# Optimization experiments

Hardware: AMD Instinct MI355X
Metric: run time of the kernel (lower is better)

The kernel has to match this reference:

```python
import jax, jax.numpy as jnp
import numpy as np

N_NODES = 50000
N_EDGES = 800000
D_IN = 128
HC = 128
D_OUT = 128
BN_EPS = 1e-5
RRELU_SLOPE = (1.0 / 8.0 + 1.0 / 3.0) / 2.0  # RReLU eval mode: (lower+upper)/2 = 11/48


def setup_inputs() -> dict:
    key = jax.random.key(0)
    ks = jax.random.split(key, 10)
    s_in = 1.0 / np.sqrt(D_IN)
    s_hc = 1.0 / np.sqrt(HC)
    return {
        "x": jax.random.normal(ks[0], (N_NODES, D_IN), jnp.float32),
        "edge_index": jax.random.randint(ks[1], (2, N_EDGES), 0, N_NODES),
        "edge_attr": jax.random.uniform(ks[2], (N_EDGES,), jnp.float32),
        # conv1: GraphConv(D_IN -> HC): lin_rel (with bias) + lin_root (no bias)
        "W1_rel": jax.random.normal(ks[3], (HC, D_IN), jnp.float32) * s_in,
        "b1": jnp.zeros((HC,), jnp.float32),
        "W1_root": jax.random.normal(ks[4], (HC, D_IN), jnp.float32) * s_in,
        # bn1 affine params
        "gamma": jnp.ones((HC,), jnp.float32),
        "beta": jnp.zeros((HC,), jnp.float32),
        # conv2: GraphConv(HC -> D_OUT)
        "W2_rel": jax.random.normal(ks[5], (D_OUT, HC), jnp.float32) * s_hc,
        "b2": jnp.zeros((D_OUT,), jnp.float32),
        "W2_root": jax.random.normal(ks[6], (D_OUT, HC), jnp.float32) * s_hc,
    }


def graph_conv(x, src, tgt, edge_w, W_rel, b_rel, W_root):
    # message: edge_weight * x[src]; aggregate: scatter-add into target nodes
    msg = x[src] * edge_w[:, None]                                   # [E, F]
    agg = jax.ops.segment_sum(msg, tgt, num_segments=x.shape[0])     # [N, F]
    return agg @ W_rel.T + b_rel + x @ W_root.T                      # [N, F_out]


def reference(x, edge_index, edge_attr, W1_rel, b1, W1_root, gamma, beta, W2_rel, b2, W2_root):
    src, tgt = edge_index[0], edge_index[1]
    h = graph_conv(x, src, tgt, edge_attr, W1_rel, b1, W1_root)      # [N, HC]
    # BatchNorm1d (training mode: biased batch stats over node dim)
    mean = h.mean(axis=0)
    var = h.var(axis=0)
    h = (h - mean) * jax.lax.rsqrt(var + BN_EPS) * gamma + beta
    # RReLU (deterministic eval slope)
    h = jnp.where(h >= 0, h, h * RRELU_SLOPE)
    return graph_conv(h, src, tgt, edge_attr, W2_rel, b2, W2_root)   # [N, D_OUT]
```

## Files before the change

kernel.cpp:

```cpp
#include <hip/hip_runtime.h>

#define N_NODES 50000
#define N_EDGES 800000
#define F 128
#define BN_EPS 1e-5f
#define SLOPE 0.22916666666666666f

#define NBKT 196
#define BKT_CAP 8192
#define P1_CHUNK 4096
#define P1_EPB 16
#define P1_BLKS 196
#define CASTX_BLKS 6250
#define CASTW_BLKS 64
#define BKT_FINAL_CAP 9984
#define REC_CAP 1160192
#define N_TILES 3125
#define GG_GRID 2048

typedef __attribute__((ext_vector_type(8))) short bf16x8;
typedef __attribute__((ext_vector_type(4))) float f32x4;
typedef unsigned long long u64;

__device__ __forceinline__ float bf2f(ushort u) {
    union { uint i; float f; } v; v.i = (uint)u << 16; return v.f;
}
__device__ __forceinline__ ushort f2bf(float f) {
    union { float f; uint i; } v; v.f = f;
    uint r = v.i + 0x7fffu + ((v.i >> 16) & 1u);
    return (ushort)(r >> 16);
}

__global__ __launch_bounds__(256) void s1p_k(const int* __restrict__ src,
        const int* __restrict__ tgt, const float* __restrict__ ew,
        int* __restrict__ bcur, u64* __restrict__ stg,
        const float* __restrict__ x, ushort* __restrict__ xb,
        const float* __restrict__ W1r, const float* __restrict__ W1t,
        const float* __restrict__ W2r, const float* __restrict__ W2t,
        ushort* __restrict__ wb) {
    const int b = blockIdx.x;
    if (b >= P1_BLKS) {
        if (b < P1_BLKS + CASTX_BLKS) {
            int i = (b - P1_BLKS) * 256 + threadIdx.x;
            float4 v = reinterpret_cast<const float4*>(x)[i];
            ushort4 o;
            o.x = f2bf(v.x); o.y = f2bf(v.y); o.z = f2bf(v.z); o.w = f2bf(v.w);
            reinterpret_cast<ushort4*>(xb)[i] = o;
        } else {
            int i = (b - P1_BLKS - CASTX_BLKS) * 256 + threadIdx.x;
            int m = i >> 12;
            int j = i & 4095;
            const float* sp = (m == 0) ? W1r : (m == 1) ? W1t : (m == 2) ? W2r : W2t;
            float4 v = reinterpret_cast<const float4*>(sp)[j];
            ushort4 o;
            o.x = f2bf(v.x); o.y = f2bf(v.y); o.z = f2bf(v.z); o.w = f2bf(v.w);
            reinterpret_cast<ushort4*>(wb)[i] = o;
        }
        return;
    }
    __shared__ uint cnt[256];
    __shared__ uint base[256];
    __shared__ uint lcur[256];
    __shared__ uint gbase[256];
    __shared__ u64 lrec[P1_CHUNK];

    const int e0 = b * P1_CHUNK;
    const int nE = min(P1_CHUNK, N_EDGES - e0);
    cnt[threadIdx.x] = 0;
    __syncthreads();

    u64 myrec[P1_EPB];
    bool myok[P1_EPB];
#pragma unroll
    for (int k = 0; k < P1_EPB; ++k) {
        int idx = threadIdx.x + (k << 8);
        bool ok = idx < nE;
        myok[k] = ok;
        if (ok) {
            int e = e0 + idx;
            uint t = (uint)tgt[e];
            uint lo = (uint)(ushort)src[e] | ((uint)f2bf(ew[e]) << 16);
            myrec[k] = (u64)lo | ((u64)t << 32);
            atomicAdd(&cnt[t >> 8], 1u);
        }
    }
    __syncthreads();
    uint v = cnt[threadIdx.x];
    base[threadIdx.x] = v;
    __syncthreads();
    for (int o = 1; o < 256; o <<= 1) {
        uint t = (threadIdx.x >= (unsigned)o) ? base[threadIdx.x - o] : 0;
        __syncthreads();
        base[threadIdx.x] += t;
        __syncthreads();
    }
    uint excl = base[threadIdx.x] - v;
    base[threadIdx.x] = excl;
    lcur[threadIdx.x] = excl;
    if (threadIdx.x < NBKT && v > 0)
        gbase[threadIdx.x] = (uint)threadIdx.x * BKT_CAP +
                             (uint)atomicAdd(&bcur[threadIdx.x], (int)v);
    __syncthreads();
#pragma unroll
    for (int k = 0; k < P1_EPB; ++k) {
        if (myok[k]) {
            uint bb = (uint)(myrec[k] >> 40);
            uint slot = atomicAdd(&lcur[bb], 1u);
            lrec[slot] = myrec[k];
        }
    }
    __syncthreads();
    for (int s = threadIdx.x; s < nE; s += 256) {
        u64 r = lrec[s];
        uint bb = (uint)(r >> 40);
        stg[gbase[bb] + ((uint)s - base[bb])] = r;
    }
}

__global__ __launch_bounds__(256) void sort2_k(const int* __restrict__ bcur,
        const u64* __restrict__ stg, uint* __restrict__ recs, int2* __restrict__ rng) {
    __shared__ int lcnt[256];
    __shared__ int lcur[256];
    __shared__ int sc[256];
    __shared__ int fbase_s;
    __shared__ uint lrec[BKT_FINAL_CAP];
    const int b = blockIdx.x;
    const int tid = threadIdx.x;

    int cnt_t = (tid < NBKT) ? bcur[tid] : 0;
    int stride_t = (tid < NBKT) ? (((cnt_t + 7) & ~7) + 1792) : 0;
    sc[tid] = stride_t;
    lcnt[tid] = 0;
    __syncthreads();
    for (int o = 1; o < 256; o <<= 1) {
        int t = (tid >= o) ? sc[tid - o] : 0;
        __syncthreads();
        sc[tid] += t;
        __syncthreads();
    }
    if (tid == b) fbase_s = sc[tid] - stride_t;
    __syncthreads();
    const int fbase = fbase_s;
    const int cnt = bcur[b];
    const u64* sb = stg + (size_t)b * BKT_CAP;

    for (int i = tid; i < cnt; i += 256)
        atomicAdd(&lcnt[(int)(sb[i] >> 32) & 255], 1);
    __syncthreads();
    const int node = b * 256 + tid;
    int myc = lcnt[tid];
    int myp = (myc + 7) & ~7;
    if (node >= N_NODES) myp = 0;
    sc[tid] = myp;
    __syncthreads();
    for (int o = 1; o < 256; o <<= 1) {
        int t = (tid >= o) ? sc[tid - o] : 0;
        __syncthreads();
        sc[tid] += t;
        __syncthreads();
    }
    const int myoff = sc[tid] - myp;
    const int ptot = sc[255];
    lcur[tid] = myoff;
    if (node < N_NODES) rng[node] = make_int2(fbase + myoff, fbase + myoff + myp);
    for (int i = tid; i < ptot; i += 256) lrec[i] = 0;
    __syncthreads();
    for (int i = tid; i < cnt; i += 256) {
        u64 r = sb[i];
        int n = (int)(r >> 32) & 255;
        int p = atomicAdd(&lcur[n], 1);
        lrec[p] = (uint)r;
    }
    __syncthreads();
    for (int i = tid; i < ptot; i += 256) recs[fbase + i] = lrec[i];
}

__global__ __launch_bounds__(256) void gg_k(const ushort* __restrict__ featb,
        const int2* __restrict__ rng, const uint* __restrict__ recs,
        const ushort* __restrict__ Wr, const ushort* __restrict__ Wt,
        const float* __restrict__ bias, float* __restrict__ out,
        ushort* __restrict__ outh, float* __restrict__ S, float* __restrict__ S2,
        int layer1) {
    __shared__ ushort As[2][16][136];

    const int lane = threadIdx.x & 63;
    const int wave = threadIdx.x >> 6;
    const int quad = lane >> 4;
    const int l16 = lane & 15;
    const int cb = wave * 32;
    const int lane2 = lane * 2;

    bf16x8 bR[2][4], bT[2][4];
#pragma unroll
    for (int t = 0; t < 2; ++t)
#pragma unroll
        for (int s = 0; s < 4; ++s) {
            int col = cb + t * 16 + l16;
            int k0 = s * 32 + quad * 8;
            bR[t][s] = *reinterpret_cast<const bf16x8*>(Wr + col * F + k0);
            bT[t][s] = *reinterpret_cast<const bf16x8*>(Wt + col * F + k0);
        }
    const float bias0 = bias[cb + l16];
    const float bias1 = bias[cb + 16 + l16];

    float s0 = 0.f, q0 = 0.f, s1 = 0.f, q1 = 0.f;
    int dbuf = 0;

    for (int tile = blockIdx.x; tile < N_TILES; tile += GG_GRID) {
        const int row0 = tile * 16;
#pragma unroll
        for (int g = 0; g < 4; ++g) {
            int node = row0 + wave * 4 + g;
            int2 r = rng[node];
            float a0 = 0.f, a1 = 0.f;
            for (int p = r.x; p < r.y; p += 8) {
                uint4 ra = *reinterpret_cast<const uint4*>(recs + p);
                uint4 rb = *reinterpret_cast<const uint4*>(recs + p + 4);
                uint u0 = *reinterpret_cast<const uint*>(featb + (size_t)(ra.x & 0xffffu) * F + lane2);
                uint u1 = *reinterpret_cast<const uint*>(featb + (size_t)(ra.y & 0xffffu) * F + lane2);
                uint u2 = *reinterpret_cast<const uint*>(featb + (size_t)(ra.z & 0xffffu) * F + lane2);
                uint u3 = *reinterpret_cast<const uint*>(featb + (size_t)(ra.w & 0xffffu) * F + lane2);
                uint u4 = *reinterpret_cast<const uint*>(featb + (size_t)(rb.x & 0xffffu) * F + lane2);
                uint u5 = *reinterpret_cast<const uint*>(featb + (size_t)(rb.y & 0xffffu) * F + lane2);
                uint u6 = *reinterpret_cast<const uint*>(featb + (size_t)(rb.z & 0xffffu) * F + lane2);
                uint u7 = *reinterpret_cast<const uint*>(featb + (size_t)(rb.w & 0xffffu) * F + lane2);
                float w0 = bf2f((ushort)(ra.x >> 16)), w1 = bf2f((ushort)(ra.y >> 16));
                float w2 = bf2f((ushort)(ra.z >> 16)), w3 = bf2f((ushort)(ra.w >> 16));
                float w4 = bf2f((ushort)(rb.x >> 16)), w5 = bf2f((ushort)(rb.y >> 16));
                float w6 = bf2f((ushort)(rb.z >> 16)), w7 = bf2f((ushort)(rb.w >> 16));
                a0 += w0 * bf2f((ushort)u0) + w1 * bf2f((ushort)u1)
                    + w2 * bf2f((ushort)u2) + w3 * bf2f((ushort)u3)
                    + w4 * bf2f((ushort)u4) + w5 * bf2f((ushort)u5)
                    + w6 * bf2f((ushort)u6) + w7 * bf2f((ushort)u7);
                a1 += w0 * bf2f((ushort)(u0 >> 16)) + w1 * bf2f((ushort)(u1 >> 16))
                    + w2 * bf2f((ushort)(u2 >> 16)) + w3 * bf2f((ushort)(u3 >> 16))
                    + w4 * bf2f((ushort)(u4 >> 16)) + w5 * bf2f((ushort)(u5 >> 16))
                    + w6 * bf2f((ushort)(u6 >> 16)) + w7 * bf2f((ushort)(u7 >> 16));
            }
            *reinterpret_cast<uint*>(&As[dbuf][wave * 4 + g][lane2]) =
                (uint)f2bf(a0) | ((uint)f2bf(a1) << 16);
        }
        __syncthreads();
        bf16x8 aR0 = *reinterpret_cast<const bf16x8*>(&As[dbuf][l16][quad * 8]);
        bf16x8 aR1 = *reinterpret_cast<const bf16x8*>(&As[dbuf][l16][quad * 8 + 32]);
        bf16x8 aR2 = *reinterpret_cast<const bf16x8*>(&As[dbuf][l16][quad * 8 + 64]);
        bf16x8 aR3 = *reinterpret_cast<const bf16x8*>(&As[dbuf][l16][quad * 8 + 96]);
        const ushort* tA = featb + (size_t)(row0 + l16) * F + quad * 8;
        bf16x8 aT0 = *reinterpret_cast<const bf16x8*>(tA);
        bf16x8 aT1 = *reinterpret_cast<const bf16x8*>(tA + 32);
        bf16x8 aT2 = *reinterpret_cast<const bf16x8*>(tA + 64);
        bf16x8 aT3 = *reinterpret_cast<const bf16x8*>(tA + 96);

        f32x4 acc0 = {0.f, 0.f, 0.f, 0.f};
        f32x4 acc1 = {0.f, 0.f, 0.f, 0.f};
        acc0 = __builtin_amdgcn_mfma_f32_16x16x32_bf16(aR0, bR[0][0], acc0, 0, 0, 0);
        acc1 = __builtin_amdgcn_mfma_f32_16x16x32_bf16(aR0, bR[1][0], acc1, 0, 0, 0);
        acc0 = __builtin_amdgcn_mfma_f32_16x16x32_bf16(aR1, bR[0][1], acc0, 0, 0, 0);
        acc1 = __builtin_amdgcn_mfma_f32_16x16x32_bf16(aR1, bR[1][1], acc1, 0, 0, 0);
        acc0 = __builtin_amdgcn_mfma_f32_16x16x32_bf16(aR2, bR[0][2], acc0, 0, 0, 0);
        acc1 = __builtin_amdgcn_mfma_f32_16x16x32_bf16(aR2, bR[1][2], acc1, 0, 0, 0);
        acc0 = __builtin_amdgcn_mfma_f32_16x16x32_bf16(aR3, bR[0][3], acc0, 0, 0, 0);
        acc1 = __builtin_amdgcn_mfma_f32_16x16x32_bf16(aR3, bR[1][3], acc1, 0, 0, 0);
        acc0 = __builtin_amdgcn_mfma_f32_16x16x32_bf16(aT0, bT[0][0], acc0, 0, 0, 0);
        acc1 = __builtin_amdgcn_mfma_f32_16x16x32_bf16(aT0, bT[1][0], acc1, 0, 0, 0);
        acc0 = __builtin_amdgcn_mfma_f32_16x16x32_bf16(aT1, bT[0][1], acc0, 0, 0, 0);
        acc1 = __builtin_amdgcn_mfma_f32_16x16x32_bf16(aT1, bT[1][1], acc1, 0, 0, 0);
        acc0 = __builtin_amdgcn_mfma_f32_16x16x32_bf16(aT2, bT[0][2], acc0, 0, 0, 0);
        acc1 = __builtin_amdgcn_mfma_f32_16x16x32_bf16(aT2, bT[1][2], acc1, 0, 0, 0);
        acc0 = __builtin_amdgcn_mfma_f32_16x16x32_bf16(aT3, bT[0][3], acc0, 0, 0, 0);
        acc1 = __builtin_amdgcn_mfma_f32_16x16x32_bf16(aT3, bT[1][3], acc1, 0, 0, 0);

        const int r0 = row0 + quad * 4;
        if (layer1) {
#pragma unroll
            for (int g = 0; g < 4; ++g) {
                float v0 = acc0[g] + bias0;
                float v1 = acc1[g] + bias1;
                outh[(r0 + g) * F + cb + l16] = f2bf(v0);
                outh[(r0 + g) * F + cb + 16 + l16] = f2bf(v1);
                s0 += v0; q0 += v0 * v0;
                s1 += v1; q1 += v1 * v1;
            }
        } else {
#pragma unroll
            for (int g = 0; g < 4; ++g) {
                out[(r0 + g) * F + cb + l16] = acc0[g] + bias0;
                out[(r0 + g) * F + cb + 16 + l16] = acc1[g] + bias1;
            }
        }
        dbuf ^= 1;
    }

    if (layer1) {
        s0 += __shfl_down(s0, 32); s0 += __shfl_down(s0, 16);
        q0 += __shfl_down(q0, 32); q0 += __shfl_down(q0, 16);
        s1 += __shfl_down(s1, 32); s1 += __shfl_down(s1, 16);
        q1 += __shfl_down(q1, 32); q1 += __shfl_down(q1, 16);
        if (lane < 16) {
            unsafeAtomicAdd(&S[cb + lane], s0);
            unsafeAtomicAdd(&S2[cb + lane], q0);
            unsafeAtomicAdd(&S[cb + 16 + lane], s1);
            unsafeAtomicAdd(&S2[cb + 16 + lane], q1);
        }
    }
}

__global__ __launch_bounds__(256) void norm_act_k(const ushort* __restrict__ hraw,
        const float* __restrict__ S, const float* __restrict__ S2,
        const float* __restrict__ gamma, const float* __restrict__ beta,
        ushort* __restrict__ hb) {
    __shared__ float sc_s[128], sh_s[128];
    if (threadIdx.x < 128) {
        int j = threadIdx.x;
        float mean = S[j] * (1.f / N_NODES);
        float var = S2[j] * (1.f / N_NODES) - mean * mean;
        float inv = rsqrtf(var + BN_EPS);
        float sc = gamma[j] * inv;
        sc_s[j] = sc;
        sh_s[j] = beta[j] - mean * sc;
    }
    __syncthreads();
    int i = blockIdx.x * 256 + threadIdx.x;
    int cbase = (i & 31) * 4;
    uint2 u = reinterpret_cast<const uint2*>(hraw)[i];
    float4 v = make_float4(bf2f((ushort)u.x), bf2f((ushort)(u.x >> 16)),
                           bf2f((ushort)u.y), bf2f((ushort)(u.y >> 16)));
    float4 sc = *reinterpret_cast<const float4*>(&sc_s[cbase]);
    float4 sh = *reinterpret_cast<const float4*>(&sh_s[cbase]);
    v.x = v.x * sc.x + sh.x;
    v.y = v.y * sc.y + sh.y;
    v.z = v.z * sc.z + sh.z;
    v.w = v.w * sc.w + sh.w;
    v.x = v.x >= 0.f ? v.x : v.x * SLOPE;
    v.y = v.y >= 0.f ? v.y : v.y * SLOPE;
    v.z = v.z >= 0.f ? v.z : v.z * SLOPE;
    v.w = v.w >= 0.f ? v.w : v.w * SLOPE;
    uint2 o;
    o.x = (uint)f2bf(v.x) | ((uint)f2bf(v.y) << 16);
    o.y = (uint)f2bf(v.z) | ((uint)f2bf(v.w) << 16);
    reinterpret_cast<uint2*>(hb)[i] = o;
}

extern "C" void kernel_launch(void* const* d_in, const int* in_sizes, int n_in,
                              void* d_out, int out_size, void* d_ws, size_t ws_size,
                              hipStream_t stream) {
    const float* x     = (const float*)d_in[0];
    const int*   ei    = (const int*)d_in[1];
    const float* ea    = (const float*)d_in[2];
    const float* W1r   = (const float*)d_in[3];
    const float* b1    = (const float*)d_in[4];
    const float* W1t   = (const float*)d_in[5];
    const float* gamma = (const float*)d_in[6];
    const float* beta  = (const float*)d_in[7];
    const float* W2r   = (const float*)d_in[8];
    const float* b2    = (const float*)d_in[9];
    const float* W2t   = (const float*)d_in[10];
    float* out = (float*)d_out;

    char* ws = (char*)d_ws;
    size_t off = 0;
    u64*    stg   = (u64*)(ws + off);    off += (size_t)NBKT * BKT_CAP * 8;
    ushort* featb = (ushort*)(ws + off); off += (size_t)N_NODES * F * 2;
    uint*   recs  = (uint*)(ws + off);   off += (size_t)REC_CAP * 4;
    int*    bcur  = (int*)(ws + off);    off += 256 * 4;
    float*  S     = (float*)(ws + off);  off += 128 * 4;
    float*  S2    = (float*)(ws + off);  off += 128 * 4;
    int2*   rng   = (int2*)(ws + off);   off += (size_t)N_NODES * 8;
    ushort* wb    = (ushort*)(ws + off); off += 4 * 16384 * 2;
    ushort* hraw  = (ushort*)d_out;

    const int* srcp = ei;
    const int* tgtp = ei + N_EDGES;

    hipMemsetAsync(bcur, 0, 256 * 4 + 256 * 4, stream);
    s1p_k<<<P1_BLKS + CASTX_BLKS + CASTW_BLKS, 256, 0, stream>>>(
        srcp, tgtp, ea, bcur, stg, x, featb, W1r, W1t, W2r, W2t, wb);
    sort2_k<<<NBKT, 256, 0, stream>>>(bcur, stg, recs, rng);

    gg_k<<<GG_GRID, 256, 0, stream>>>(featb, rng, recs, wb, wb + 16384, b1,
                                      out, hraw, S, S2, 1);
    norm_act_k<<<CASTX_BLKS, 256, 0, stream>>>(hraw, S, S2, gamma, beta, featb);
    gg_k<<<GG_GRID, 256, 0, stream>>>(featb, rng, recs, wb + 32768, wb + 49152, b2,
                                      out, hraw, S, S2, 0);
}
```

Baseline: 265.1 us.

## Split fused gather+GEMM into separate gather and MFMA GEMM kernels

Unfuses the per-layer gather-aggregate and MFMA GEMM into two kernels. A gather kernel writes aggregated bf16 rows into a scratch buffer that reuses the staging area. A GEMM kernel on a smaller persistent grid then reads those rows plus the root features. The aim is to drop the block-wide barrier and LDS staging, and let the irregular gather run at full occupancy without weight registers held for the MFMA. The cost is an extra global round trip of the aggregated matrix and two more launches.

```diff
diff --git a/kernel.cpp b/kernel.cpp
--- a/kernel.cpp
+++ b/kernel.cpp
@@ -15,8 +15,8 @@
 #define CASTW_BLKS 64
 #define BKT_FINAL_CAP 9984
 #define REC_CAP 1160192
-#define N_TILES 3125
-#define GG_GRID 2048
+#define N_RT 3125
+#define GEMM_GRID 512
 
 typedef __attribute__((ext_vector_type(8))) short bf16x8;
 typedef __attribute__((ext_vector_type(4))) float f32x4;
@@ -175,20 +175,51 @@
     for (int i = tid; i < ptot; i += 256) recs[fbase + i] = lrec[i];
 }
 
-__global__ __launch_bounds__(256) void gg_k(const ushort* __restrict__ featb,
+__global__ __launch_bounds__(256) void gather_k(const ushort* __restrict__ featb,
         const int2* __restrict__ rng, const uint* __restrict__ recs,
-        const ushort* __restrict__ Wr, const ushort* __restrict__ Wt,
-        const float* __restrict__ bias, float* __restrict__ out,
-        ushort* __restrict__ outh, float* __restrict__ S, float* __restrict__ S2,
-        int layer1) {
-    __shared__ ushort As[2][16][136];
-
+        ushort* __restrict__ aggb) {
+    int node = blockIdx.x * 4 + (threadIdx.x >> 6);
+    int lane2 = (threadIdx.x & 63) * 2;
+    int2 r = rng[node];
+    float a0 = 0.f, a1 = 0.f;
+    for (int p = r.x; p < r.y; p += 8) {
+        uint4 ra = *reinterpret_cast<const uint4*>(recs + p);
+        uint4 rb = *reinterpret_cast<const uint4*>(recs + p + 4);
+        uint u0 = *reinterpret_cast<const uint*>(featb + (size_t)(ra.x & 0xffffu) * F + lane2);
+        uint u1 = *reinterpret_cast<const uint*>(featb + (size_t)(ra.y & 0xffffu) * F + lane2);
+        uint u2 = *reinterpret_cast<const uint*>(featb + (size_t)(ra.z & 0xffffu) * F + lane2);
+        uint u3 = *reinterpret_cast<const uint*>(featb + (size_t)(ra.w & 0xffffu) * F + lane2);
+        uint u4 = *reinterpret_cast<const uint*>(featb + (size_t)(rb.x & 0xffffu) * F + lane2);
+        uint u5 = *reinterpret_cast<const uint*>(featb + (size_t)(rb.y & 0xffffu) * F + lane2);
+        uint u6 = *reinterpret_cast<const uint*>(featb + (size_t)(rb.z & 0xffffu) * F + lane2);
+        uint u7 = *reinterpret_cast<const uint*>(featb + (size_t)(rb.w & 0xffffu) * F + lane2);
+        float w0 = bf2f((ushort)(ra.x >> 16)), w1 = bf2f((ushort)(ra.y >> 16));
+        float w2 = bf2f((ushort)(ra.z >> 16)), w3 = bf2f((ushort)(ra.w >> 16));
+        float w4 = bf2f((ushort)(rb.x >> 16)), w5 = bf2f((ushort)(rb.y >> 16));
+        float w6 = bf2f((ushort)(rb.z >> 16)), w7 = bf2f((ushort)(rb.w >> 16));
+        a0 += w0 * bf2f((ushort)u0) + w1 * bf2f((ushort)u1)
+            + w2 * bf2f((ushort)u2) + w3 * bf2f((ushort)u3)
+            + w4 * bf2f((ushort)u4) + w5 * bf2f((ushort)u5)
+            + w6 * bf2f((ushort)u6) + w7 * bf2f((ushort)u7);
+        a1 += w0 * bf2f((ushort)(u0 >> 16)) + w1 * bf2f((ushort)(u1 >> 16))
+            + w2 * bf2f((ushort)(u2 >> 16)) + w3 * bf2f((ushort)(u3 >> 16))
+            + w4 * bf2f((ushort)(u4 >> 16)) + w5 * bf2f((ushort)(u5 >> 16))
+            + w6 * bf2f((ushort)(u6 >> 16)) + w7 * bf2f((ushort)(u7 >> 16));
+    }
+    *reinterpret_cast<uint*>(aggb + (size_t)node * F + lane2) =
+        (uint)f2bf(a0) | ((uint)f2bf(a1) << 16);
+}
+
+__global__ __launch_bounds__(256) void gemm_mfma(const ushort* __restrict__ R,
+        const ushort* __restrict__ T, const ushort* __restrict__ Wr,
+        const ushort* __restrict__ Wt, const float* __restrict__ bias,
+        float* __restrict__ out, ushort* __restrict__ outh,
+        float* __restrict__ S, float* __restrict__ S2, int fuse_bn) {
     const int lane = threadIdx.x & 63;
     const int wave = threadIdx.x >> 6;
     const int quad = lane >> 4;
     const int l16 = lane & 15;
     const int cb = wave * 32;
-    const int lane2 = lane * 2;
 
     bf16x8 bR[2][4], bT[2][4];
 #pragma unroll
@@ -204,48 +235,15 @@
     const float bias1 = bias[cb + 16 + l16];
 
     float s0 = 0.f, q0 = 0.f, s1 = 0.f, q1 = 0.f;
-    int dbuf = 0;
-
-    for (int tile = blockIdx.x; tile < N_TILES; tile += GG_GRID) {
-        const int row0 = tile * 16;
-#pragma unroll
-        for (int g = 0; g < 4; ++g) {
-            int node = row0 + wave * 4 + g;
-            int2 r = rng[node];
-            float a0 = 0.f, a1 = 0.f;
-            for (int p = r.x; p < r.y; p += 8) {
-                uint4 ra = *reinterpret_cast<const uint4*>(recs + p);
-                uint4 rb = *reinterpret_cast<const uint4*>(recs + p + 4);
-                uint u0 = *reinterpret_cast<const uint*>(featb + (size_t)(ra.x & 0xffffu) * F + lane2);
-                uint u1 = *reinterpret_cast<const uint*>(featb + (size_t)(ra.y & 0xffffu) * F + lane2);
-                uint u2 = *reinterpret_cast<const uint*>(featb + (size_t)(ra.z & 0xffffu) * F + lane2);
-                uint u3 = *reinterpret_cast<const uint*>(featb + (size_t)(ra.w & 0xffffu) * F + lane2);
-                uint u4 = *reinterpret_cast<const uint*>(featb + (size_t)(rb.x & 0xffffu) * F + lane2);
-                uint u5 = *reinterpret_cast<const uint*>(featb + (size_t)(rb.y & 0xffffu) * F + lane2);
-                uint u6 = *reinterpret_cast<const uint*>(featb + (size_t)(rb.z & 0xffffu) * F + lane2);
-                uint u7 = *reinterpret_cast<const uint*>(featb + (size_t)(rb.w & 0xffffu) * F + lane2);
-                float w0 = bf2f((ushort)(ra.x >> 16)), w1 = bf2f((ushort)(ra.y >> 16));
-                float w2 = bf2f((ushort)(ra.z >> 16)), w3 = bf2f((ushort)(ra.w >> 16));
-                float w4 = bf2f((ushort)(rb.x >> 16)), w5 = bf2f((ushort)(rb.y >> 16));
-                float w6 = bf2f((ushort)(rb.z >> 16)), w7 = bf2f((ushort)(rb.w >> 16));
-                a0 += w0 * bf2f((ushort)u0) + w1 * bf2f((ushort)u1)
-                    + w2 * bf2f((ushort)u2) + w3 * bf2f((ushort)u3)
-                    + w4 * bf2f((ushort)u4) + w5 * bf2f((ushort)u5)
-                    + w6 * bf2f((ushort)u6) + w7 * bf2f((ushort)u7);
-                a1 += w0 * bf2f((ushort)(u0 >> 16)) + w1 * bf2f((ushort)(u1 >> 16))
-                    + w2 * bf2f((ushort)(u2 >> 16)) + w3 * bf2f((ushort)(u3 >> 16))
-                    + w4 * bf2f((ushort)(u4 >> 16)) + w5 * bf2f((ushort)(u5 >> 16))
-                    + w6 * bf2f((ushort)(u6 >> 16)) + w7 * bf2f((ushort)(u7 >> 16));
-            }
-            *reinterpret_cast<uint*>(&As[dbuf][wave * 4 + g][lane2]) =
-                (uint)f2bf(a0) | ((uint)f2bf(a1) << 16);
-        }
-        __syncthreads();
-        bf16x8 aR0 = *reinterpret_cast<const bf16x8*>(&As[dbuf][l16][quad * 8]);
-        bf16x8 aR1 = *reinterpret_cast<const bf16x8*>(&As[dbuf][l16][quad * 8 + 32]);
-        bf16x8 aR2 = *reinterpret_cast<const bf16x8*>(&As[dbuf][l16][quad * 8 + 64]);
-        bf16x8 aR3 = *reinterpret_cast<const bf16x8*>(&As[dbuf][l16][quad * 8 + 96]);
-        const ushort* tA = featb + (size_t)(row0 + l16) * F + quad * 8;
+
+    for (int rt = blockIdx.x; rt < N_RT; rt += GEMM_GRID) {
+        const int row0 = rt * 16;
+        const ushort* rA = R + (row0 + l16) * F + quad * 8;
+        const ushort* tA = T + (row0 + l16) * F + quad * 8;
+        bf16x8 aR0 = *reinterpret_cast<const bf16x8*>(rA);
+        bf16x8 aR1 = *reinterpret_cast<const bf16x8*>(rA + 32);
+        bf16x8 aR2 = *reinterpret_cast<const bf16x8*>(rA + 64);
+        bf16x8 aR3 = *reinterpret_cast<const bf16x8*>(rA + 96);
         bf16x8 aT0 = *reinterpret_cast<const bf16x8*>(tA);
         bf16x8 aT1 = *reinterpret_cast<const bf16x8*>(tA + 32);
         bf16x8 aT2 = *reinterpret_cast<const bf16x8*>(tA + 64);
@@ -271,7 +269,7 @@
         acc1 = __builtin_amdgcn_mfma_f32_16x16x32_bf16(aT3, bT[1][3], acc1, 0, 0, 0);
 
         const int r0 = row0 + quad * 4;
-        if (layer1) {
+        if (fuse_bn) {
 #pragma unroll
             for (int g = 0; g < 4; ++g) {
                 float v0 = acc0[g] + bias0;
@@ -288,10 +286,9 @@
                 out[(r0 + g) * F + cb + 16 + l16] = acc1[g] + bias1;
             }
         }
-        dbuf ^= 1;
-    }
-
-    if (layer1) {
+    }
+
+    if (fuse_bn) {
         s0 += __shfl_down(s0, 32); s0 += __shfl_down(s0, 16);
         q0 += __shfl_down(q0, 32); q0 += __shfl_down(q0, 16);
         s1 += __shfl_down(s1, 32); s1 += __shfl_down(s1, 16);
@@ -367,6 +364,7 @@
     float*  S2    = (float*)(ws + off);  off += 128 * 4;
     int2*   rng   = (int2*)(ws + off);   off += (size_t)N_NODES * 8;
     ushort* wb    = (ushort*)(ws + off); off += 4 * 16384 * 2;
+    ushort* aggb  = (ushort*)stg;
     ushort* hraw  = (ushort*)d_out;
 
     const int* srcp = ei;
@@ -377,9 +375,11 @@
         srcp, tgtp, ea, bcur, stg, x, featb, W1r, W1t, W2r, W2t, wb);
     sort2_k<<<NBKT, 256, 0, stream>>>(bcur, stg, recs, rng);
 
-    gg_k<<<GG_GRID, 256, 0, stream>>>(featb, rng, recs, wb, wb + 16384, b1,
-                                      out, hraw, S, S2, 1);
+    gather_k<<<N_NODES / 4, 256, 0, stream>>>(featb, rng, recs, aggb);
+    gemm_mfma<<<GEMM_GRID, 256, 0, stream>>>(aggb, featb, wb, wb + 16384, b1,
+                                             out, hraw, S, S2, 1);
     norm_act_k<<<CASTX_BLKS, 256, 0, stream>>>(hraw, S, S2, gamma, beta, featb);
-    gg_k<<<GG_GRID, 256, 0, stream>>>(featb, rng, recs, wb + 32768, wb + 49152, b2,
-                                      out, hraw, S, S2, 0);
-}
+    gather_k<<<N_NODES / 4, 256, 0, stream>>>(featb, rng, recs, aggb);
+    gemm_mfma<<<GEMM_GRID, 256, 0, stream>>>(aggb, featb, wb + 32768, wb + 49152, b2,
+                                             out, hraw, S, S2, 0);
+}
```

After: 231.1 us. -12.8%, faster.
